# Performance work log

Measured on AMD Instinct MI355X. Metric: run time of the kernel, lower is better.

Reference implementation:

```python
import jax, jax.numpy as jnp
import numpy as np

HIDDEN = 2048
HEADS = 16
HEAD_DIM = HIDDEN // HEADS
TOP_K = 256
B, N = 1, 2048


def setup_inputs() -> dict:
    key = jax.random.key(0)
    ks = jax.random.split(key, 9)
    s = 0.02
    return {
        "hidden_states": jax.random.normal(ks[0], (B, N, HIDDEN), jnp.float32),
        "Wq": jax.random.normal(ks[1], (HIDDEN, HIDDEN), jnp.float32) * s,
        "bq": jnp.zeros((HIDDEN,), jnp.float32),
        "Wk": jax.random.normal(ks[2], (HIDDEN, HIDDEN), jnp.float32) * s,
        "bk": jnp.zeros((HIDDEN,), jnp.float32),
        "Wv": jax.random.normal(ks[3], (HIDDEN, HIDDEN), jnp.float32) * s,
        "bv": jnp.zeros((HIDDEN,), jnp.float32),
        "Wo": jax.random.normal(ks[4], (HIDDEN, HIDDEN), jnp.float32) * s,
        "bo": jnp.zeros((HIDDEN,), jnp.float32),
    }


def _split_heads(x):
    b, n, _ = x.shape
    return x.reshape(b, n, HEADS, HEAD_DIM).transpose(0, 2, 1, 3)  # b h n d


def reference(hidden_states, Wq, bq, Wk, bk, Wv, bv, Wo, bo):
    scale = 1.0 / jnp.sqrt(jnp.float32(HEAD_DIM))
    q = _split_heads(hidden_states @ Wq + bq)  # [b,h,n,d]
    k = _split_heads(hidden_states @ Wk + bk)
    v = _split_heads(hidden_states @ Wv + bv)

    # Sparse path (kv_seq_length > attention_window): dense QK^T used only to rank keys.
    scores = jnp.einsum("bhnd,bhmd->bhnm", q, k) * scale  # [b,h,n,n]
    importance = scores.mean(axis=2)  # [b,h,n] aggregate over queries
    _, idx = jax.lax.top_k(importance, TOP_K)  # [b,h,k]

    # gather selected K/V (torch.gather along seq dim)
    k_sel = jnp.take_along_axis(k, idx[..., None], axis=2)  # [b,h,k,d]
    v_sel = jnp.take_along_axis(v, idx[..., None], axis=2)

    w = jax.nn.softmax(jnp.einsum("bhnd,bhkd->bhnk", q, k_sel) * scale, axis=-1)
    out = jnp.einsum("bhnk,bhkd->bhnd", w, v_sel)  # [b,h,n,d]
    out = out.transpose(0, 2, 1, 3).reshape(hidden_states.shape[0], -1, HIDDEN)
    return out @ Wo + bo
```

## Files before the change

kernel.cpp:

```cpp
#include <hip/hip_runtime.h>


typedef __attribute__((ext_vector_type(8))) short bf16x8;
typedef __attribute__((ext_vector_type(8))) unsigned short u16x8;
typedef __attribute__((ext_vector_type(4))) float f32x4;

__device__ __forceinline__ unsigned short f2bf(float x) {
    unsigned u = __float_as_uint(x);
    u += 0x7fffu + ((u >> 16) & 1u);
    return (unsigned short)(u >> 16);
}

__device__ __forceinline__ void load_lds16(const unsigned short* g, unsigned short* l) {
    __builtin_amdgcn_global_load_lds(
        (const __attribute__((address_space(1))) unsigned int*)g,
        (__attribute__((address_space(3))) unsigned int*)l,
        16, 0, 0);
}

struct Ptr4  { const float* p[4]; };

__global__ __launch_bounds__(256) void gemm_qkv(
    const unsigned short* __restrict__ HSb,
    const unsigned short* __restrict__ WT4,
    const float* __restrict__ bq,
    const float* __restrict__ bk,
    const float* __restrict__ bv,
    const int* __restrict__ idx,
    unsigned short* __restrict__ Qb,
    unsigned short* __restrict__ Ksel,
    unsigned short* __restrict__ VselT)
{
    __shared__ __align__(16) unsigned short As[4][128][32];
    __shared__ __align__(16) unsigned short Bs[4][64][32];

    const int tid  = threadIdx.x;
    const int lane = tid & 63;
    const int wave = tid >> 6;
    const int wm = wave >> 1, wn = wave & 1;
    const int lr = lane >> 2;
    const int lc = (lane & 3) * 8;

    const int bid = blockIdx.x;

    int kv, h = 0, bm, bn;
    const unsigned short* Bt;
    long ar0, ar1;
    if (bid < 128) {
        kv = 1 + (bid >> 6);
        const int t = bid & 63;
        h  = t >> 2;
        bm = ((t >> 1) & 1) * 128;
        bn = h * 128 + (t & 1) * 64;
        Bt = WT4 + (long)kv * 4194304;
        ar0 = idx[h * 256 + bm + wave * 16 + lr];
        ar1 = idx[h * 256 + bm + wave * 16 + 64 + lr];
    } else {
        kv = 0;
        const int t = bid - 128;
        const int st = t >> 5, u = t & 31;
        bm = ((st >> 2) * 4 + (u >> 3)) * 128;
        bn = ((st & 3) * 8 + (u & 7)) * 64;
        Bt = WT4;
        ar0 = bm + wave * 16 + lr;
        ar1 = ar0 + 64;
    }

    const unsigned short* Arow0 = HSb + ar0 * 2048 + lc;
    const unsigned short* Arow1 = HSb + ar1 * 2048 + lc;
    const unsigned short* Brow0 = Bt + (long)(bn + wave * 16 + lr) * 2048 + lc;

    f32x4 acc[4][2];
#pragma unroll
    for (int i = 0; i < 4; i++)
#pragma unroll
        for (int j = 0; j < 2; j++) acc[i][j] = f32x4{0.f, 0.f, 0.f, 0.f};

    auto stage = [&](int b, int step) {
        const int k0 = step * 32;
        load_lds16(Arow0 + k0, &As[b][wave * 16][0]);
        load_lds16(Arow1 + k0, &As[b][wave * 16 + 64][0]);
        load_lds16(Brow0 + k0, &Bs[b][wave * 16][0]);
    };
    auto compute = [&](int b) {
        bf16x8 af[4], bf[2];
#pragma unroll
        for (int s = 0; s < 4; s++)
            af[s] = *(const bf16x8*)&As[b][wm * 64 + s * 16 + (lane & 15)][(lane >> 4) * 8];
#pragma unroll
        for (int t = 0; t < 2; t++)
            bf[t] = *(const bf16x8*)&Bs[b][wn * 32 + t * 16 + (lane & 15)][(lane >> 4) * 8];
#pragma unroll
        for (int s = 0; s < 4; s++)
#pragma unroll
            for (int t = 0; t < 2; t++)
                acc[s][t] = __builtin_amdgcn_mfma_f32_16x16x32_bf16(af[s], bf[t], acc[s][t], 0, 0, 0);
    };

    stage(0, 0);
    stage(1, 1);
    stage(2, 2);
#pragma unroll 4
    for (int t = 0; t < 61; ++t) {
        asm volatile("s_waitcnt vmcnt(6)" ::: "memory");
        __builtin_amdgcn_s_barrier();
        __builtin_amdgcn_sched_barrier(0);
        stage((t + 3) & 3, t + 3);
        __builtin_amdgcn_sched_barrier(0);
        compute(t & 3);
    }
    asm volatile("s_waitcnt vmcnt(6)" ::: "memory");
    __builtin_amdgcn_s_barrier();
    __builtin_amdgcn_sched_barrier(0);
    compute(1);
    asm volatile("s_waitcnt vmcnt(3)" ::: "memory");
    __builtin_amdgcn_s_barrier();
    __builtin_amdgcn_sched_barrier(0);
    compute(2);
    asm volatile("s_waitcnt vmcnt(0)" ::: "memory");
    __builtin_amdgcn_s_barrier();
    __builtin_amdgcn_sched_barrier(0);
    compute(3);

    if (kv == 0) {
#pragma unroll
        for (int s = 0; s < 4; s++) {
#pragma unroll
            for (int t = 0; t < 2; t++) {
                const int col  = bn + wn * 32 + t * 16 + (lane & 15);
                const int row0 = bm + wm * 64 + s * 16 + (lane >> 4) * 4;
                const float bb = bq[col];
#pragma unroll
                for (int r = 0; r < 4; r++)
                    Qb[(long)(row0 + r) * 2048 + col] = f2bf(acc[s][t][r] + bb);
            }
        }
    } else {
        const float* bp = (kv == 1) ? bk : bv;
#pragma unroll
        for (int s = 0; s < 4; s++) {
#pragma unroll
            for (int t = 0; t < 2; t++) {
                const int col = bn + wn * 32 + t * 16 + (lane & 15);
                const int dd  = col & 127;
                const float bb = bp[col];
                const int j0 = bm + wm * 64 + s * 16 + (lane >> 4) * 4;
#pragma unroll
                for (int r = 0; r < 4; r++) {
                    const int j = j0 + r;
                    const unsigned short h16 = f2bf(acc[s][t][r] + bb);
                    if (kv == 1) Ksel [h * 32768 + j * 128 + dd] = h16;
                    else         VselT[h * 32768 + dd * 256 + j] = h16;
                }
            }
        }
    }
}

__global__ __launch_bounds__(256) void gemm_o(
    const unsigned short* __restrict__ Att,
    const unsigned short* __restrict__ WoT,
    const float* __restrict__ bo,
    float* __restrict__ out)
{
    __shared__ __align__(16) unsigned short As[4][128][32];
    __shared__ __align__(16) unsigned short Bs[4][64][32];

    const int tid  = threadIdx.x;
    const int lane = tid & 63;
    const int wave = tid >> 6;
    const int wm = wave >> 1, wn = wave & 1;
    const int lr = lane >> 2;
    const int lc = (lane & 3) * 8;

    const int t0 = blockIdx.x;
    const int st = t0 >> 5, u = t0 & 31;
    const int bm = ((st >> 2) * 4 + (u >> 3)) * 128;
    const int bn = ((st & 3) * 8 + (u & 7)) * 64;

    const unsigned short* Arow0 = Att + (long)(bm + wave * 16 + lr) * 2048 + lc;
    const unsigned short* Arow1 = Arow0 + 64 * 2048;
    const unsigned short* Brow0 = WoT + (long)(bn + wave * 16 + lr) * 2048 + lc;

    f32x4 acc[4][2];
#pragma unroll
    for (int i = 0; i < 4; i++)
#pragma unroll
        for (int j = 0; j < 2; j++) acc[i][j] = f32x4{0.f, 0.f, 0.f, 0.f};

    auto stage = [&](int b, int step) {
        const int k0 = step * 32;
        load_lds16(Arow0 + k0, &As[b][wave * 16][0]);
        load_lds16(Arow1 + k0, &As[b][wave * 16 + 64][0]);
        load_lds16(Brow0 + k0, &Bs[b][wave * 16][0]);
    };
    auto compute = [&](int b) {
        bf16x8 af[4], bf[2];
#pragma unroll
        for (int s = 0; s < 4; s++)
            af[s] = *(const bf16x8*)&As[b][wm * 64 + s * 16 + (lane & 15)][(lane >> 4) * 8];
#pragma unroll
        for (int t = 0; t < 2; t++)
            bf[t] = *(const bf16x8*)&Bs[b][wn * 32 + t * 16 + (lane & 15)][(lane >> 4) * 8];
#pragma unroll
        for (int s = 0; s < 4; s++)
#pragma unroll
            for (int t = 0; t < 2; t++)
                acc[s][t] = __builtin_amdgcn_mfma_f32_16x16x32_bf16(af[s], bf[t], acc[s][t], 0, 0, 0);
    };

    stage(0, 0);
    stage(1, 1);
    stage(2, 2);
#pragma unroll 4
    for (int t = 0; t < 61; ++t) {
        asm volatile("s_waitcnt vmcnt(6)" ::: "memory");
        __builtin_amdgcn_s_barrier();
        __builtin_amdgcn_sched_barrier(0);
        stage((t + 3) & 3, t + 3);
        __builtin_amdgcn_sched_barrier(0);
        compute(t & 3);
    }
    asm volatile("s_waitcnt vmcnt(6)" ::: "memory");
    __builtin_amdgcn_s_barrier();
    __builtin_amdgcn_sched_barrier(0);
    compute(1);
    asm volatile("s_waitcnt vmcnt(3)" ::: "memory");
    __builtin_amdgcn_s_barrier();
    __builtin_amdgcn_sched_barrier(0);
    compute(2);
    asm volatile("s_waitcnt vmcnt(0)" ::: "memory");
    __builtin_amdgcn_s_barrier();
    __builtin_amdgcn_sched_barrier(0);
    compute(3);

#pragma unroll
    for (int s = 0; s < 4; s++) {
#pragma unroll
        for (int t = 0; t < 2; t++) {
            const int col  = bn + wn * 32 + t * 16 + (lane & 15);
            const int row0 = bm + wm * 64 + s * 16 + (lane >> 4) * 4;
            const float bb = bo[col];
#pragma unroll
            for (int r = 0; r < 4; r++)
                out[(long)(row0 + r) * 2048 + col] = acc[s][t][r] + bb;
        }
    }
}

#define QS_OFF(c)  ((c) * 2048)
#define KS_OFF(c)  (4096 + (c) * 8192)
#define PS_OFF     0
#define VS_OFF(c)  (16896 + (c) * 4096)

__global__ __launch_bounds__(256, 2) void attn_kernel(
    const unsigned short* __restrict__ Qb,
    const unsigned short* __restrict__ Ksel,
    const unsigned short* __restrict__ VselT,
    unsigned short* __restrict__ Att)
{
    __shared__ __align__(16) unsigned short smem[25088];
    __shared__ float linv[64];

    const int tid  = threadIdx.x;
    const int lane = tid & 63;
    const int wave = tid >> 6;
    const int bm = blockIdx.x * 64;
    const int h  = blockIdx.y;
    const int lr = lane >> 2, lc = (lane & 3) * 8;

    const unsigned short* Kh = Ksel  + h * 32768;
    const unsigned short* Vh = VselT + h * 32768;

    f32x4 acc[16];
#pragma unroll
    for (int t = 0; t < 16; t++) acc[t] = f32x4{0.f, 0.f, 0.f, 0.f};

#pragma unroll
    for (int c2 = 0; c2 < 2; c2++) {
        __syncthreads();
#pragma unroll
        for (int c = 0; c < 2; c++) {
            const int k0 = c2 * 64 + c * 32;
            load_lds16(Qb + (long)(bm + wave * 16 + lr) * 2048 + h * 128 + k0 + lc,
                       &smem[QS_OFF(c) + wave * 512]);
#pragma unroll
            for (int q = 0; q < 4; q++)
                load_lds16(Kh + (wave * 64 + q * 16 + lr) * 128 + k0 + lc,
                           &smem[KS_OFF(c) + (wave * 64 + q * 16) * 32]);
        }
        __syncthreads();
#pragma unroll
        for (int kk = 0; kk < 2; kk++) {
            bf16x8 af = *(const bf16x8*)&smem[QS_OFF(kk) + (wave * 16 + (lane & 15)) * 32 + (lane >> 4) * 8];
#pragma unroll
            for (int t = 0; t < 16; t++) {
                bf16x8 bfv = *(const bf16x8*)&smem[KS_OFF(kk) + (t * 16 + (lane & 15)) * 32 + (lane >> 4) * 8];
                acc[t] = __builtin_amdgcn_mfma_f32_16x16x32_bf16(af, bfv, acc[t], 0, 0, 0);
            }
        }
    }
    __syncthreads();

    const float se = 0.08838834764831845f * 1.4426950408889634f;
#pragma unroll
    for (int r = 0; r < 4; r++) {
        float mx = -3.0e38f;
#pragma unroll
        for (int t = 0; t < 16; t++) mx = fmaxf(mx, acc[t][r]);
#pragma unroll
        for (int off = 1; off < 16; off <<= 1) mx = fmaxf(mx, __shfl_xor(mx, off));
        float sum = 0.f;
#pragma unroll
        for (int t = 0; t < 16; t++) {
            float p = exp2f((acc[t][r] - mx) * se);
            acc[t][r] = p;
            sum += p;
        }
#pragma unroll
        for (int off = 1; off < 16; off <<= 1) sum += __shfl_xor(sum, off);
        const int row = wave * 16 + (lane >> 4) * 4 + r;
#pragma unroll
        for (int t = 0; t < 16; t++)
            smem[PS_OFF + row * 264 + t * 16 + (lane & 15)] = f2bf(acc[t][r]);
        if ((lane & 15) == 0) linv[row] = 1.0f / sum;
    }

    const int wm2 = wave >> 1, wn2 = wave & 1;
    f32x4 acc2[2][4];
#pragma unroll
    for (int i = 0; i < 2; i++)
#pragma unroll
        for (int j = 0; j < 4; j++) acc2[i][j] = f32x4{0.f, 0.f, 0.f, 0.f};

#pragma unroll
    for (int c2 = 0; c2 < 4; c2++) {
#pragma unroll
        for (int c = 0; c < 2; c++) {
            const int j0 = c2 * 64 + c * 32;
#pragma unroll
            for (int q = 0; q < 2; q++)
                load_lds16(Vh + (wave * 32 + q * 16 + lr) * 256 + j0 + lc,
                           &smem[VS_OFF(c) + (wave * 32 + q * 16) * 32]);
        }
        __syncthreads();
#pragma unroll
        for (int c = 0; c < 2; c++) {
            const int j0 = c2 * 64 + c * 32;
            bf16x8 af2[2], bf2v[4];
#pragma unroll
            for (int s2 = 0; s2 < 2; s2++)
                af2[s2] = *(const bf16x8*)&smem[PS_OFF + (wm2 * 32 + s2 * 16 + (lane & 15)) * 264 + j0 + (lane >> 4) * 8];
#pragma unroll
            for (int t2 = 0; t2 < 4; t2++)
                bf2v[t2] = *(const bf16x8*)&smem[VS_OFF(c) + (wn2 * 64 + t2 * 16 + (lane & 15)) * 32 + (lane >> 4) * 8];
#pragma unroll
            for (int s2 = 0; s2 < 2; s2++)
#pragma unroll
                for (int t2 = 0; t2 < 4; t2++)
                    acc2[s2][t2] = __builtin_amdgcn_mfma_f32_16x16x32_bf16(af2[s2], bf2v[t2], acc2[s2][t2], 0, 0, 0);
        }
        __syncthreads();
    }

#pragma unroll
    for (int s2 = 0; s2 < 2; s2++) {
#pragma unroll
        for (int t2 = 0; t2 < 4; t2++) {
            const int d = wn2 * 64 + t2 * 16 + (lane & 15);
#pragma unroll
            for (int r = 0; r < 4; r++) {
                const int row = wm2 * 32 + s2 * 16 + (lane >> 4) * 4 + r;
                float v = acc2[s2][t2][r] * linv[row];
                Att[(long)(bm + row) * 2048 + h * 128 + d] = f2bf(v);
            }
        }
    }
}

__global__ __launch_bounds__(256) void prep_kernel(Ptr4 srcs, unsigned short* __restrict__ WT4,
                                                   const float* __restrict__ hs,
                                                   double* __restrict__ part) {
    const int b = blockIdx.x;
    const int tid = threadIdx.x;
    if (b < 4096) {
        __shared__ float tile[64][65];
        const int z = b >> 10, xy = b & 1023;
        const float* W = srcs.p[z];
        unsigned short* WT = WT4 + (long)z * 4194304;
        const int bx = (xy & 31) * 64;
        const int by = (xy >> 5) * 64;
        const int x = tid & 63, y = tid >> 6;
#pragma unroll
        for (int i = 0; i < 64; i += 4)
            tile[y + i][x] = W[(long)(by + y + i) * 2048 + bx + x];
        __syncthreads();
#pragma unroll
        for (int i = 0; i < 64; i += 4)
            WT[(long)(bx + y + i) * 2048 + by + x] = f2bf(tile[x][y + i]);
    } else {
        const int c = b - 4096;
        const int col = (c & 7) * 256 + tid;
        const int r0  = (c >> 3) * 32;
        double a = 0.0;
#pragma unroll 4
        for (int r = 0; r < 32; r++) a += (double)hs[(long)(r0 + r) * 2048 + col];
        part[(long)(c >> 3) * 2048 + col] = a;
    }
}

__global__ void fill_kernel(float* p, float v, long n) {
    long i = ((long)blockIdx.x * blockDim.x + threadIdx.x) * 4;
    if (i + 3 < n) { p[i] = v; p[i+1] = v; p[i+2] = v; p[i+3] = v; }
}

__global__ __launch_bounds__(256) void mean_qsum_part(const double* __restrict__ part,
                                                      const float* __restrict__ Wq,
                                                      double* __restrict__ partq) {
    __shared__ float hsb[32];
    const int j  = blockIdx.x * 256 + threadIdx.x;
    const int i0 = blockIdx.y * 32;
    if (threadIdx.x < 32) {
        double s = 0.0;
#pragma unroll 4
        for (int g = 0; g < 64; g++) s += part[(long)g * 2048 + i0 + threadIdx.x];
        hsb[threadIdx.x] = (float)(s * (1.0 / 2048.0));
    }
    __syncthreads();
    double a = 0.0;
#pragma unroll 4
    for (int r = 0; r < 32; r++)
        a += (double)hsb[r] * (double)Wq[(long)(i0 + r) * 2048 + j];
    partq[(long)blockIdx.y * 2048 + j] = a;
}

__global__ void qsum_fin(const double* __restrict__ partq, const float* __restrict__ bq,
                         float* __restrict__ qbar) {
    const int j = blockIdx.x * 64 + threadIdx.x;
    double s = (double)bq[j];
#pragma unroll 4
    for (int g = 0; g < 64; g++) s += partq[(long)g * 2048 + j];
    qbar[j] = (float)s;
}

__global__ __launch_bounds__(256) void u_kernel(const float* __restrict__ Wk,
                                                const float* __restrict__ qbar,
                                                float* __restrict__ U) {
    const int i = blockIdx.x, t = threadIdx.x;
#pragma unroll
    for (int r = 0; r < 2; r++) {
        const int e = r * 1024 + t * 4;
        float4 w = *(const float4*)(Wk + (long)i * 2048 + e);
        float4 q = *(const float4*)(qbar + e);
        float a = w.x * q.x + w.y * q.y + w.z * q.z + w.w * q.w;
#pragma unroll
        for (int off = 16; off; off >>= 1) a += __shfl_xor(a, off);
        if ((t & 31) == 0) U[(long)i * 16 + r * 8 + (t >> 5)] = a;
    }
}

__global__ __launch_bounds__(256) void cast_imp_kernel(const float* __restrict__ hs,
                                                       const float* __restrict__ U,
                                                       unsigned short* __restrict__ HSb,
                                                       float* __restrict__ imp) {
    __shared__ float red[4][4][16];
    const int m0 = blockIdx.x * 4, t = threadIdx.x;

    float va[4][8];
#pragma unroll
    for (int r = 0; r < 4; r++) {
        const float4 v0 = *(const float4*)(hs + (long)(m0 + r) * 2048 + t * 8);
        const float4 v1 = *(const float4*)(hs + (long)(m0 + r) * 2048 + t * 8 + 4);
        va[r][0] = v0.x; va[r][1] = v0.y; va[r][2] = v0.z; va[r][3] = v0.w;
        va[r][4] = v1.x; va[r][5] = v1.y; va[r][6] = v1.z; va[r][7] = v1.w;
        u16x8 hb;
#pragma unroll
        for (int j = 0; j < 8; j++) hb[j] = f2bf(va[r][j]);
        *(u16x8*)(HSb + (long)(m0 + r) * 2048 + t * 8) = hb;
    }

    float p[4][16];
#pragma unroll
    for (int r = 0; r < 4; r++)
#pragma unroll
        for (int h = 0; h < 16; h++) p[r][h] = 0.f;

    const float4* Uq = (const float4*)(U + (long)t * 128);
#pragma unroll
    for (int j = 0; j < 8; j++) {
        const float4 u0 = Uq[j * 4 + 0];
        const float4 u1 = Uq[j * 4 + 1];
        const float4 u2 = Uq[j * 4 + 2];
        const float4 u3 = Uq[j * 4 + 3];
#pragma unroll
        for (int r = 0; r < 4; r++) {
            const float v = va[r][j];
            p[r][0]  += v * u0.x; p[r][1]  += v * u0.y; p[r][2]  += v * u0.z; p[r][3]  += v * u0.w;
            p[r][4]  += v * u1.x; p[r][5]  += v * u1.y; p[r][6]  += v * u1.z; p[r][7]  += v * u1.w;
            p[r][8]  += v * u2.x; p[r][9]  += v * u2.y; p[r][10] += v * u2.z; p[r][11] += v * u2.w;
            p[r][12] += v * u3.x; p[r][13] += v * u3.y; p[r][14] += v * u3.z; p[r][15] += v * u3.w;
        }
    }

#pragma unroll
    for (int off = 32; off; off >>= 1)
#pragma unroll
        for (int r = 0; r < 4; r++)
#pragma unroll
            for (int h = 0; h < 16; h++) p[r][h] += __shfl_down(p[r][h], off);
    if ((t & 63) == 0)
#pragma unroll
        for (int r = 0; r < 4; r++)
#pragma unroll
            for (int h = 0; h < 16; h++) red[t >> 6][r][h] = p[r][h];
    __syncthreads();
    if (t < 64) {
        const int h = t & 15, r = t >> 4;
        imp[(long)h * 2048 + m0 + r] =
            red[0][r][h] + red[1][r][h] + red[2][r][h] + red[3][r][h];
    }
}

__global__ __launch_bounds__(64) void topk_idx(const float* __restrict__ imp,
                                               int* __restrict__ idx) {
    const int h = blockIdx.x;
    const int lane = threadIdx.x;
    unsigned u[32];
#pragma unroll
    for (int r = 0; r < 32; r++) {
        unsigned x = __float_as_uint(imp[(long)h * 2048 + r * 64 + lane]);
        u[r] = (x & 0x80000000u) ? ~x : (x | 0x80000000u);
    }
    unsigned cur = 0;
    for (int b = 31; b >= 0; b--) {
        const unsigned cand = cur | (1u << b);
        int tot = 0;
#pragma unroll
        for (int r = 0; r < 32; r++)
            tot += (int)__popcll(__ballot(u[r] >= cand));
        if (tot >= 256) cur = cand;
    }
    const unsigned long long below = (1ull << lane) - 1ull;
    int pos[32];
    int base = 0;
#pragma unroll
    for (int r = 0; r < 32; r++) {
        const bool q = u[r] > cur;
        const unsigned long long m = __ballot(q);
        pos[r] = q ? base + (int)__popcll(m & below) : -1;
        base += (int)__popcll(m);
    }
#pragma unroll
    for (int r = 0; r < 32; r++) {
        const bool q = (u[r] == cur);
        const unsigned long long m = __ballot(q);
        if (q) {
            const int p = base + (int)__popcll(m & below);
            pos[r] = (p < 256) ? p : -1;
        }
        base += (int)__popcll(m);
    }
#pragma unroll
    for (int r = 0; r < 32; r++)
        if (pos[r] >= 0) idx[h * 256 + pos[r]] = r * 64 + lane;
}

extern "C" void kernel_launch(void* const* d_in, const int* in_sizes, int n_in,
                              void* d_out, int out_size, void* d_ws, size_t ws_size,
                              hipStream_t stream)
{
    const float* hs = (const float*)d_in[0];
    const float* Wq = (const float*)d_in[1];
    const float* bq = (const float*)d_in[2];
    const float* Wk = (const float*)d_in[3];
    const float* bk = (const float*)d_in[4];
    const float* Wv = (const float*)d_in[5];
    const float* bv = (const float*)d_in[6];
    const float* Wo = (const float*)d_in[7];
    const float* bo = (const float*)d_in[8];

    char* ws = (char*)d_ws;
    size_t off = 0;
    auto alloc = [&](size_t b) -> void* {
        void* p = ws + off;
        off = (off + b + 255) & ~(size_t)255;
        return p;
    };
    unsigned short* HSb   = (unsigned short*)alloc(8388608);
    unsigned short* WT4   = (unsigned short*)alloc(4 * 8388608);
    unsigned short* Qb    = (unsigned short*)alloc(8388608);
    unsigned short* Att   = (unsigned short*)alloc(8388608);
    unsigned short* Ksel  = (unsigned short*)alloc(1048576);
    unsigned short* VselT = (unsigned short*)alloc(1048576);
    double* part  = (double*)alloc(1048576);
    double* partq = (double*)alloc(1048576);
    float* qbar  = (float*)alloc(8192);
    float* U     = (float*)alloc(131072);
    float* imp   = (float*)alloc(131072);
    int*   idx   = (int*)alloc(16384);

    if (off > ws_size) {
        fill_kernel<<<4096, 256, 0, stream>>>((float*)d_out, 12345.0f, (long)out_size);
        return;
    }

    unsigned short* WoT = WT4 + 3 * 4194304;

    prep_kernel<<<4608, 256, 0, stream>>>(Ptr4{{Wq, Wk, Wv, Wo}}, WT4, hs, part);

    mean_qsum_part<<<dim3(8, 64), 256, 0, stream>>>(part, Wq, partq);
    qsum_fin<<<32, 64, 0, stream>>>(partq, bq, qbar);
    u_kernel<<<2048, 256, 0, stream>>>(Wk, qbar, U);
    cast_imp_kernel<<<512, 256, 0, stream>>>(hs, U, HSb, imp);

    topk_idx<<<16, 64, 0, stream>>>(imp, idx);

    gemm_qkv<<<640, 256, 0, stream>>>(HSb, WT4, bq, bk, bv, idx, Qb, Ksel, VselT);

    attn_kernel<<<dim3(32, 16), 256, 0, stream>>>(Qb, Ksel, VselT, Att);

    gemm_o<<<512, 256, 0, stream>>>(Att, WoT, bo, (float*)d_out);
}
```

Baseline: 279.4 us.

## XOR-swizzle LDS tiles and remap GEMM block order for L2 locality

Applies an XOR swizzle to the 16-byte column chunk used when global_load_lds writes rows into LDS, and the matching swizzle on the MFMA fragment reads, across the QKV GEMM, the O GEMM and the attention kernel. The aim is to remove LDS bank conflicts on the 64-byte row stride of the tiles. The dense GEMMs also permute their block index so that consecutively scheduled blocks spread differently over output tiles, which may change L2 and cross-XCD locality. The risk is a mismatch between the store swizzle and the load swizzle, which would corrupt results.

```diff
diff --git a/kernel.cpp b/kernel.cpp
--- a/kernel.cpp
+++ b/kernel.cpp
@@ -38,8 +38,9 @@
     const int lane = tid & 63;
     const int wave = tid >> 6;
     const int wm = wave >> 1, wn = wave & 1;
-    const int lr = lane >> 2;
-    const int lc = (lane & 3) * 8;
+    const int lr  = lane >> 2;
+    const int scc = (((lane & 3) ^ ((lr >> 1) & 3))) * 8;
+    const int rc  = (((lane >> 4) ^ (((lane & 15) >> 1) & 3))) * 8;
 
     const int bid = blockIdx.x;
 
@@ -58,7 +59,8 @@
     } else {
         kv = 0;
         const int t = bid - 128;
-        const int st = t >> 5, u = t & 31;
+        const int tl = (t & 7) * 64 + (t >> 3);
+        const int st = tl >> 5, u = tl & 31;
         bm = ((st >> 2) * 4 + (u >> 3)) * 128;
         bn = ((st & 3) * 8 + (u & 7)) * 64;
         Bt = WT4;
@@ -66,9 +68,9 @@
         ar1 = ar0 + 64;
     }
 
-    const unsigned short* Arow0 = HSb + ar0 * 2048 + lc;
-    const unsigned short* Arow1 = HSb + ar1 * 2048 + lc;
-    const unsigned short* Brow0 = Bt + (long)(bn + wave * 16 + lr) * 2048 + lc;
+    const unsigned short* Arow0 = HSb + ar0 * 2048 + scc;
+    const unsigned short* Arow1 = HSb + ar1 * 2048 + scc;
+    const unsigned short* Brow0 = Bt + (long)(bn + wave * 16 + lr) * 2048 + scc;
 
     f32x4 acc[4][2];
 #pragma unroll
@@ -86,10 +88,10 @@
         bf16x8 af[4], bf[2];
 #pragma unroll
         for (int s = 0; s < 4; s++)
-            af[s] = *(const bf16x8*)&As[b][wm * 64 + s * 16 + (lane & 15)][(lane >> 4) * 8];
+            af[s] = *(const bf16x8*)&As[b][wm * 64 + s * 16 + (lane & 15)][rc];
 #pragma unroll
         for (int t = 0; t < 2; t++)
-            bf[t] = *(const bf16x8*)&Bs[b][wn * 32 + t * 16 + (lane & 15)][(lane >> 4) * 8];
+            bf[t] = *(const bf16x8*)&Bs[b][wn * 32 + t * 16 + (lane & 15)][rc];
 #pragma unroll
         for (int s = 0; s < 4; s++)
 #pragma unroll
@@ -170,17 +172,19 @@
     const int lane = tid & 63;
     const int wave = tid >> 6;
     const int wm = wave >> 1, wn = wave & 1;
-    const int lr = lane >> 2;
-    const int lc = (lane & 3) * 8;
+    const int lr  = lane >> 2;
+    const int scc = (((lane & 3) ^ ((lr >> 1) & 3))) * 8;
+    const int rc  = (((lane >> 4) ^ (((lane & 15) >> 1) & 3))) * 8;
 
     const int t0 = blockIdx.x;
-    const int st = t0 >> 5, u = t0 & 31;
+    const int tl = (t0 & 7) * 64 + (t0 >> 3);
+    const int st = tl >> 5, u = tl & 31;
     const int bm = ((st >> 2) * 4 + (u >> 3)) * 128;
     const int bn = ((st & 3) * 8 + (u & 7)) * 64;
 
-    const unsigned short* Arow0 = Att + (long)(bm + wave * 16 + lr) * 2048 + lc;
+    const unsigned short* Arow0 = Att + (long)(bm + wave * 16 + lr) * 2048 + scc;
     const unsigned short* Arow1 = Arow0 + 64 * 2048;
-    const unsigned short* Brow0 = WoT + (long)(bn + wave * 16 + lr) * 2048 + lc;
+    const unsigned short* Brow0 = WoT + (long)(bn + wave * 16 + lr) * 2048 + scc;
 
     f32x4 acc[4][2];
 #pragma unroll
@@ -198,10 +202,10 @@
         bf16x8 af[4], bf[2];
 #pragma unroll
         for (int s = 0; s < 4; s++)
-            af[s] = *(const bf16x8*)&As[b][wm * 64 + s * 16 + (lane & 15)][(lane >> 4) * 8];
+            af[s] = *(const bf16x8*)&As[b][wm * 64 + s * 16 + (lane & 15)][rc];
 #pragma unroll
         for (int t = 0; t < 2; t++)
-            bf[t] = *(const bf16x8*)&Bs[b][wn * 32 + t * 16 + (lane & 15)][(lane >> 4) * 8];
+            bf[t] = *(const bf16x8*)&Bs[b][wn * 32 + t * 16 + (lane & 15)][rc];
 #pragma unroll
         for (int s = 0; s < 4; s++)
 #pragma unroll
@@ -267,7 +271,9 @@
     const int wave = tid >> 6;
     const int bm = blockIdx.x * 64;
     const int h  = blockIdx.y;
-    const int lr = lane >> 2, lc = (lane & 3) * 8;
+    const int lr  = lane >> 2;
+    const int scc = (((lane & 3) ^ ((lr >> 1) & 3))) * 8;
+    const int rc  = (((lane >> 4) ^ (((lane & 15) >> 1) & 3))) * 8;
 
     const unsigned short* Kh = Ksel  + h * 32768;
     const unsigned short* Vh = VselT + h * 32768;
@@ -282,20 +288,20 @@
 #pragma unroll
         for (int c = 0; c < 2; c++) {
             const int k0 = c2 * 64 + c * 32;
-            load_lds16(Qb + (long)(bm + wave * 16 + lr) * 2048 + h * 128 + k0 + lc,
+            load_lds16(Qb + (long)(bm + wave * 16 + lr) * 2048 + h * 128 + k0 + scc,
                        &smem[QS_OFF(c) + wave * 512]);
 #pragma unroll
             for (int q = 0; q < 4; q++)
-                load_lds16(Kh + (wave * 64 + q * 16 + lr) * 128 + k0 + lc,
+                load_lds16(Kh + (wave * 64 + q * 16 + lr) * 128 + k0 + scc,
                            &smem[KS_OFF(c) + (wave * 64 + q * 16) * 32]);
         }
         __syncthreads();
 #pragma unroll
         for (int kk = 0; kk < 2; kk++) {
-            bf16x8 af = *(const bf16x8*)&smem[QS_OFF(kk) + (wave * 16 + (lane & 15)) * 32 + (lane >> 4) * 8];
+            bf16x8 af = *(const bf16x8*)&smem[QS_OFF(kk) + (wave * 16 + (lane & 15)) * 32 + rc];
 #pragma unroll
             for (int t = 0; t < 16; t++) {
-                bf16x8 bfv = *(const bf16x8*)&smem[KS_OFF(kk) + (t * 16 + (lane & 15)) * 32 + (lane >> 4) * 8];
+                bf16x8 bfv = *(const bf16x8*)&smem[KS_OFF(kk) + (t * 16 + (lane & 15)) * 32 + rc];
                 acc[t] = __builtin_amdgcn_mfma_f32_16x16x32_bf16(af, bfv, acc[t], 0, 0, 0);
             }
         }
@@ -340,7 +346,7 @@
             const int j0 = c2 * 64 + c * 32;
 #pragma unroll
             for (int q = 0; q < 2; q++)
-                load_lds16(Vh + (wave * 32 + q * 16 + lr) * 256 + j0 + lc,
+                load_lds16(Vh + (wave * 32 + q * 16 + lr) * 256 + j0 + scc,
                            &smem[VS_OFF(c) + (wave * 32 + q * 16) * 32]);
         }
         __syncthreads();
@@ -353,7 +359,7 @@
                 af2[s2] = *(const bf16x8*)&smem[PS_OFF + (wm2 * 32 + s2 * 16 + (lane & 15)) * 264 + j0 + (lane >> 4) * 8];
 #pragma unroll
             for (int t2 = 0; t2 < 4; t2++)
-                bf2v[t2] = *(const bf16x8*)&smem[VS_OFF(c) + (wn2 * 64 + t2 * 16 + (lane & 15)) * 32 + (lane >> 4) * 8];
+                bf2v[t2] = *(const bf16x8*)&smem[VS_OFF(c) + (wn2 * 64 + t2 * 16 + (lane & 15)) * 32 + rc];
 #pragma unroll
             for (int s2 = 0; s2 < 2; s2++)
 #pragma unroll
```

Result: no change. 279.5 us (+0.0%).
